# Performance work log

Measured on AMD Instinct MI355X. Metric: run time of the kernel, lower is better.

The kernel has to match this reference:

```python
import jax, jax.numpy as jnp
import numpy as np

B, T, D = 2, 2048, 2048
H, KVH = 32, 8
HD = D // H            # 64
G = H // KVH           # 4


def setup_inputs() -> dict:
    key = jax.random.key(0)
    k1, k2, k3 = jax.random.split(key, 3)
    x_q = jax.random.normal(k1, (B, T, D), dtype=jnp.float32)
    W_qkv = jax.random.normal(k2, (D, H * HD + 2 * KVH * HD), dtype=jnp.float32) * 0.02
    W_out = jax.random.normal(k3, (D, D), dtype=jnp.float32) * 0.02
    b_out = jnp.zeros((D,), dtype=jnp.float32)
    # real rotary tables: theta = 10000^{-2i/HD}
    inv_freq = 1.0 / (10000.0 ** (np.arange(0, HD, 2) / HD))   # [HD/2]
    pos = np.arange(T)[:, None] * inv_freq[None, :]            # [T, HD/2]
    rope_cos = jnp.asarray(np.cos(pos), dtype=jnp.float32)
    rope_sin = jnp.asarray(np.sin(pos), dtype=jnp.float32)
    return {"x_q": x_q, "W_qkv": W_qkv, "W_out": W_out, "b_out": b_out,
            "rope_cos": rope_cos, "rope_sin": rope_sin}


def _apply_rope(x, cos, sin):
    # x: [B, h, T, HD], cos/sin: [T, HD/2] -> interleaved even/odd rotation
    xe = x[..., 0::2]
    xo = x[..., 1::2]
    c = cos[None, None, :, :]
    s = sin[None, None, :, :]
    return jnp.stack([xe * c - xo * s, xe * s + xo * c], axis=-1).reshape(x.shape)


def reference(x_q, W_qkv, W_out, b_out, rope_cos, rope_sin):
    b, t, d = x_q.shape
    qkv = x_q @ W_qkv                                  # [B,T,3072]
    q_lin = qkv[..., : H * HD]
    k_lin = qkv[..., H * HD: H * HD + KVH * HD]
    v_lin = qkv[..., H * HD + KVH * HD:]
    q = q_lin.reshape(b, t, H, HD).transpose(0, 2, 1, 3)        # [B,H,T,HD]
    k = k_lin.reshape(b, t, KVH, HD).transpose(0, 2, 1, 3)      # [B,KVH,T,HD]
    v = v_lin.reshape(b, t, KVH, HD).transpose(0, 2, 1, 3)
    # GQA expand (repeat_interleave over heads)
    k = jnp.repeat(k, G, axis=1)                                # [B,H,T,HD]
    v = jnp.repeat(v, G, axis=1)
    q = _apply_rope(q, rope_cos[:t], rope_sin[:t])
    k = _apply_rope(k, rope_cos[:t], rope_sin[:t])
    scale = 1.0 / jnp.sqrt(jnp.asarray(HD, dtype=x_q.dtype))
    logits = jnp.einsum('bhqd,bhkd->bhqk', q, k) * scale        # [B,H,T,T]
    causal = jnp.triu(jnp.ones((t, t), dtype=bool), 1)[None, None]
    logits = jnp.where(causal, jnp.finfo(logits.dtype).min, logits)
    attn = jax.nn.softmax(logits, axis=-1)
    out = jnp.einsum('bhqk,bhkd->bhqd', attn, v)                # [B,H,T,HD]
    out = out.transpose(0, 2, 1, 3).reshape(b, t, H * HD)       # [B,T,D]
    out = out @ W_out + b_out
    return jnp.nan_to_num(out, nan=0.0, posinf=1e4, neginf=-1e4)
```

## Files before the change

kernel.cpp:

```cpp
#include <hip/hip_runtime.h>
#include <hip/hip_bf16.h>

#define DI __device__ __forceinline__

#if __has_builtin(__builtin_amdgcn_exp2f)
#define EXP2(x) __builtin_amdgcn_exp2f(x)
#else
#define EXP2(x) exp2f(x)
#endif

namespace {

constexpr int Bc = 2, Tc = 2048, Dc = 2048, Hc = 32, KVHc = 8, HDc = 64;
constexpr int NQKV = Hc * HDc + 2 * KVHc * HDc;

typedef __bf16 bf16x8 __attribute__((ext_vector_type(8)));
typedef unsigned short u16x8 __attribute__((ext_vector_type(8)));
typedef unsigned short u16x4 __attribute__((ext_vector_type(4)));
typedef float f32x4 __attribute__((ext_vector_type(4)));

union FragU { u16x8 u; bf16x8 b; u16x4 h[2]; };

DI float bits2f(unsigned int u) {
  union { unsigned int i; float f; } v; v.i = u << 16; return v.f;
}
DI unsigned short f2bits(float f) {
  __hip_bfloat16 h = __float2bfloat16(f);
  return *reinterpret_cast<unsigned short*>(&h);
}

DI void store_out(float* p, float v) { *p = v; }
DI void store_out(__hip_bfloat16* p, float v) { *p = __float2bfloat16(v); }

typedef __attribute__((address_space(1))) void gv_t;
typedef __attribute__((address_space(3))) void lv_t;

template<int ROWB, int TOTB, bool SWZ = false>
DI void stage_tile(const char* g, long long row_stride_b, char* lds) {
  const int tid = threadIdx.x;
  const int wid = tid >> 6, lane = tid & 63;
#pragma unroll
  for (int it = 0; it < TOTB / 4096; ++it) {
    int off = it * 4096 + wid * 1024 + lane * 16;
    int row = off / ROWB;
    int colb = off % ROWB;
    if (SWZ) colb ^= (row & 7) << 4;
    const char* gp = g + (long long)row * row_stride_b + colb;
    char* lp = lds + it * 4096 + wid * 1024;
    __builtin_amdgcn_global_load_lds((gv_t*)gp, (lv_t*)lp, 16, 0, 0);
  }
}

__global__ __launch_bounds__(256) void cvt_f32_bf16(
    const float* __restrict__ in, __hip_bfloat16* __restrict__ out) {
  const long long i = ((long long)blockIdx.x * 256 + threadIdx.x) * 8;
  const float4 a = *(const float4*)(in + i);
  const float4 b = *(const float4*)(in + i + 4);
  u16x8 r;
  r[0] = f2bits(a.x); r[1] = f2bits(a.y); r[2] = f2bits(a.z); r[3] = f2bits(a.w);
  r[4] = f2bits(b.x); r[5] = f2bits(b.y); r[6] = f2bits(b.z); r[7] = f2bits(b.w);
  *(u16x8*)((unsigned short*)out + i) = r;
}

__global__ __launch_bounds__(256) void transpose_cvt_kernel(
    const float* __restrict__ in, __hip_bfloat16* __restrict__ out, int R, int C) {
  __shared__ unsigned short tile[64][65];
  const int c0 = blockIdx.x * 64, r0 = blockIdx.y * 64;
  const int tid = threadIdx.x;
  const int rr = tid >> 2, seg = (tid & 3) * 16;
  const float* src = in + (long long)(r0 + rr) * C + c0 + seg;
#pragma unroll
  for (int i = 0; i < 16; ++i) tile[rr][seg + i] = f2bits(src[i]);
  __syncthreads();
  unsigned short* dst = (unsigned short*)out + (long long)(c0 + rr) * R + r0 + seg;
#pragma unroll
  for (int i = 0; i < 16; ++i) dst[i] = tile[seg + i][rr];
}

__global__ __launch_bounds__(256) void transpose_kernel(
    const __hip_bfloat16* __restrict__ in, __hip_bfloat16* __restrict__ out,
    int R, int C) {
  __shared__ unsigned short tile[64][65];
  const long long slice = (long long)R * C;
  const unsigned short* ip = (const unsigned short*)in + (long long)blockIdx.z * slice;
  unsigned short* op = (unsigned short*)out + (long long)blockIdx.z * slice;
  const int c0 = blockIdx.x * 64, r0 = blockIdx.y * 64;
  const int tid = threadIdx.x;
  const int rr = tid >> 2, seg = (tid & 3) * 16;
  const unsigned short* src = ip + (long long)(r0 + rr) * C + c0 + seg;
#pragma unroll
  for (int i = 0; i < 16; ++i) tile[rr][seg + i] = src[i];
  __syncthreads();
  unsigned short* dst = op + (long long)(c0 + rr) * R + r0 + seg;
#pragma unroll
  for (int i = 0; i < 16; ++i) dst[i] = tile[seg + i][rr];
}

template <typename OT>
__global__ __launch_bounds__(256) void gemm_bt(
    const __hip_bfloat16* __restrict__ A, const __hip_bfloat16* __restrict__ Bt,
    const float* __restrict__ bias, OT* __restrict__ C, int M, int N, int K) {
  __shared__ __align__(16) char As[8192];
  __shared__ __align__(16) char Bs[8192];
  const int n0 = blockIdx.x * 128;
  const int m0 = blockIdx.y * 128;
  const int tid = threadIdx.x;
  const int wid = tid >> 6, lane = tid & 63;
  const int wm = (wid >> 1) * 64, wn = (wid & 1) * 64;
  const int l15 = lane & 15, quad = lane >> 4;

  f32x4 acc[4][4] = {};

  const int nk = K >> 5;
  for (int kt = 0; kt < nk; ++kt) {
    __syncthreads();
    stage_tile<64, 8192>((const char*)(A + (long long)m0 * K + kt * 32), (long long)K * 2, As);
    stage_tile<64, 8192>((const char*)(Bt + (long long)n0 * K + kt * 32), (long long)K * 2, Bs);
    __syncthreads();

    FragU a[4], b[4];
#pragma unroll
    for (int mt = 0; mt < 4; ++mt)
      a[mt].u = *(const u16x8*)(As + ((wm + mt * 16 + l15) * 32 + quad * 8) * 2);
#pragma unroll
    for (int nt = 0; nt < 4; ++nt)
      b[nt].u = *(const u16x8*)(Bs + ((wn + nt * 16 + l15) * 32 + quad * 8) * 2);
#pragma unroll
    for (int mt = 0; mt < 4; ++mt)
#pragma unroll
      for (int nt = 0; nt < 4; ++nt)
        acc[mt][nt] = __builtin_amdgcn_mfma_f32_16x16x32_bf16(a[mt].b, b[nt].b, acc[mt][nt], 0, 0, 0);
  }

#pragma unroll
  for (int nt = 0; nt < 4; ++nt) {
    const int col = n0 + wn + nt * 16 + l15;
    const float bv = bias ? bias[col] : 0.f;
#pragma unroll
    for (int mt = 0; mt < 4; ++mt) {
#pragma unroll
      for (int r = 0; r < 4; ++r) {
        const int row = m0 + wm + mt * 16 + quad * 4 + r;
        store_out(C + (long long)row * N + col, acc[mt][nt][r] + bv);
      }
    }
  }
}

__global__ __launch_bounds__(384) void rope_reshape(
    const __hip_bfloat16* __restrict__ qkv, const float* __restrict__ cosb,
    const float* __restrict__ sinb, __hip_bfloat16* __restrict__ Qo,
    __hip_bfloat16* __restrict__ Ko, __hip_bfloat16* __restrict__ Vo) {
  constexpr float SCL = 0.125f * 1.44269504088896f;
  const int row = blockIdx.x;
  const int b = row / Tc, t = row % Tc;
  const unsigned short* src = (const unsigned short*)qkv + (long long)row * NQKV;
  const float* cb = cosb + t * 32;
  const float* sb = sinb + t * 32;
  const int e = (int)threadIdx.x * 8;
  const u16x8 v = *(const u16x8*)(src + e);
  if (e < Hc * HDc) {
    const int hh = e >> 6, d = e & 63, ii = d >> 1;
    u16x8 r;
#pragma unroll
    for (int p = 0; p < 4; ++p) {
      const float c = cb[ii + p], s = sb[ii + p];
      const float xe = bits2f(v[2 * p]), xo = bits2f(v[2 * p + 1]);
      r[2 * p] = f2bits((xe * c - xo * s) * SCL);
      r[2 * p + 1] = f2bits((xe * s + xo * c) * SCL);
    }
    const long long idx = (((long long)b * Hc + hh) * Tc + t) * HDc + d;
    *(u16x8*)((unsigned short*)Qo + idx) = r;
  } else if (e < Hc * HDc + KVHc * HDc) {
    const int e2 = e - Hc * HDc;
    const int kh = e2 >> 6, d = e2 & 63, ii = d >> 1;
    u16x8 r;
#pragma unroll
    for (int p = 0; p < 4; ++p) {
      const float c = cb[ii + p], s = sb[ii + p];
      const float xe = bits2f(v[2 * p]), xo = bits2f(v[2 * p + 1]);
      r[2 * p] = f2bits(xe * c - xo * s);
      r[2 * p + 1] = f2bits(xe * s + xo * c);
    }
    const long long idx = (((long long)b * KVHc + kh) * Tc + t) * HDc + d;
    *(u16x8*)((unsigned short*)Ko + idx) = r;
  } else {
    const int e2 = e - (Hc * HDc + KVHc * HDc);
    const int kh = e2 >> 6, d = e2 & 63;
    const long long idx = (((long long)b * KVHc + kh) * Tc + t) * HDc + d;
    *(u16x8*)((unsigned short*)Vo + idx) = v;
  }
}


DI void mask_diag(f32x4 (&S)[4], int wid, int l15, int quad) {
#pragma unroll
  for (int nt = 0; nt < 4; ++nt)
#pragma unroll
    for (int r = 0; r < 4; ++r)
      if ((nt * 16 + quad * 4 + r) > (wid * 16 + l15)) S[nt][r] = -1e30f;
}

DI float softmax_pack(f32x4 (&S)[4], float& m_i, float& l_i, FragU (&pa)[2]) {
  float mx = fmaxf(fmaxf(S[0][0], S[0][1]), fmaxf(S[0][2], S[0][3]));
#pragma unroll
  for (int nt = 1; nt < 4; ++nt)
    mx = fmaxf(mx, fmaxf(fmaxf(S[nt][0], S[nt][1]), fmaxf(S[nt][2], S[nt][3])));
  mx = fmaxf(mx, __shfl_xor(mx, 16, 64));
  mx = fmaxf(mx, __shfl_xor(mx, 32, 64));
  const float mnew = fmaxf(m_i, mx);
  const float alpha = EXP2(m_i - mnew);
  m_i = mnew;
  float sum = 0.f;
#pragma unroll
  for (int nt = 0; nt < 4; ++nt)
#pragma unroll
    for (int r = 0; r < 4; ++r) {
      const float pp = EXP2(S[nt][r] - mnew);
      S[nt][r] = pp;
      sum += pp;
    }
  sum += __shfl_xor(sum, 16, 64);
  sum += __shfl_xor(sum, 32, 64);
  l_i = l_i * alpha + sum;
#pragma unroll
  for (int ks = 0; ks < 2; ++ks)
#pragma unroll
    for (int r = 0; r < 4; ++r) {
      pa[ks].u[r] = f2bits(S[2 * ks][r]);
      pa[ks].u[4 + r] = f2bits(S[2 * ks + 1][r]);
    }
  return alpha;
}

DI void attn_tile(const char* __restrict__ Ksb, const char* __restrict__ Vsb,
                  const FragU (&qa)[2], f32x4 (&O)[4], float& m_i, float& l_i,
                  bool diag, int wid, int l15, int quad, int sw) {
  f32x4 S[4] = {};
  __builtin_amdgcn_s_setprio(1);
#pragma unroll
  for (int nt = 0; nt < 4; ++nt) {
#pragma unroll
    for (int ks = 0; ks < 2; ++ks) {
      FragU kb;
      kb.u = *(const u16x8*)(Ksb + (nt * 16 + l15) * 128 + ((((ks << 2) | quad) ^ sw) << 4));
      S[nt] = __builtin_amdgcn_mfma_f32_16x16x32_bf16(kb.b, qa[ks].b, S[nt], 0, 0, 0);
    }
  }
  __builtin_amdgcn_s_setprio(0);
  if (diag) mask_diag(S, wid, l15, quad);
  FragU pa[2];
  const float alpha = softmax_pack(S, m_i, l_i, pa);
#pragma unroll
  for (int nt = 0; nt < 4; ++nt)
#pragma unroll
    for (int r = 0; r < 4; ++r) O[nt][r] *= alpha;
  __builtin_amdgcn_s_setprio(1);
#pragma unroll
  for (int nt = 0; nt < 4; ++nt) {
    const char* vrow = Vsb + (nt * 16 + l15) * 128 + ((quad & 1) << 3);
    const int gq = quad >> 1;
#pragma unroll
    for (int ks = 0; ks < 2; ++ks) {
      FragU vb;
      vb.h[0] = *(const u16x4*)(vrow + (((ks * 4 + gq) ^ sw) << 4));
      vb.h[1] = *(const u16x4*)(vrow + (((ks * 4 + gq + 2) ^ sw) << 4));
      O[nt] = __builtin_amdgcn_mfma_f32_16x16x32_bf16(vb.b, pa[ks].b, O[nt], 0, 0, 0);
    }
  }
  __builtin_amdgcn_s_setprio(0);
}

DI void attn_tile_dual(const char* __restrict__ Ksb, const char* __restrict__ Vsb,
                       const FragU (&qaB)[2], const FragU (&qaA)[2],
                       f32x4 (&OB)[4], f32x4 (&OA)[4],
                       float& mB, float& lB, float& mA, float& lA,
                       bool diagA, int wid, int l15, int quad, int sw) {
  f32x4 SB[4] = {}, SA[4] = {};
  __builtin_amdgcn_s_setprio(1);
#pragma unroll
  for (int nt = 0; nt < 4; ++nt) {
#pragma unroll
    for (int ks = 0; ks < 2; ++ks) {
      FragU kb;
      kb.u = *(const u16x8*)(Ksb + (nt * 16 + l15) * 128 + ((((ks << 2) | quad) ^ sw) << 4));
      SB[nt] = __builtin_amdgcn_mfma_f32_16x16x32_bf16(kb.b, qaB[ks].b, SB[nt], 0, 0, 0);
      SA[nt] = __builtin_amdgcn_mfma_f32_16x16x32_bf16(kb.b, qaA[ks].b, SA[nt], 0, 0, 0);
    }
  }
  __builtin_amdgcn_s_setprio(0);
  if (diagA) mask_diag(SA, wid, l15, quad);
  FragU paB[2], paA[2];
  const float aB = softmax_pack(SB, mB, lB, paB);
  const float aA = softmax_pack(SA, mA, lA, paA);
#pragma unroll
  for (int nt = 0; nt < 4; ++nt)
#pragma unroll
    for (int r = 0; r < 4; ++r) {
      OB[nt][r] *= aB;
      OA[nt][r] *= aA;
    }
  __builtin_amdgcn_s_setprio(1);
#pragma unroll
  for (int nt = 0; nt < 4; ++nt) {
    const char* vrow = Vsb + (nt * 16 + l15) * 128 + ((quad & 1) << 3);
    const int gq = quad >> 1;
#pragma unroll
    for (int ks = 0; ks < 2; ++ks) {
      FragU vb;
      vb.h[0] = *(const u16x4*)(vrow + (((ks * 4 + gq) ^ sw) << 4));
      vb.h[1] = *(const u16x4*)(vrow + (((ks * 4 + gq + 2) ^ sw) << 4));
      OB[nt] = __builtin_amdgcn_mfma_f32_16x16x32_bf16(vb.b, paB[ks].b, OB[nt], 0, 0, 0);
      OA[nt] = __builtin_amdgcn_mfma_f32_16x16x32_bf16(vb.b, paA[ks].b, OA[nt], 0, 0, 0);
    }
  }
  __builtin_amdgcn_s_setprio(0);
}

__global__ __launch_bounds__(256, 4) void attn_kernel(
    const __hip_bfloat16* __restrict__ Q, const __hip_bfloat16* __restrict__ K,
    const __hip_bfloat16* __restrict__ Vt, __hip_bfloat16* __restrict__ Out) {
  __shared__ __align__(16) char Ks[2][8192];
  __shared__ __align__(16) char Vs[2][8192];

  const int p = blockIdx.x;
  const int qtA = p, qtB = (Tc / 64 - 1) - p;
  const int h = blockIdx.y, b = blockIdx.z;
  const int kvh = h >> 2;
  const int tid = threadIdx.x, wid = tid >> 6, lane = tid & 63;
  const int l15 = lane & 15, quad = lane >> 4;
  const int sw = l15 & 7;

  const char* QgA = (const char*)(Q + (((long long)b * Hc + h) * Tc + qtA * 64) * HDc);
  const char* QgB = (const char*)(Q + (((long long)b * Hc + h) * Tc + qtB * 64) * HDc);
  const char* Kg = (const char*)(K + (((long long)b * KVHc + kvh) * Tc) * HDc);
  const char* Vg = (const char*)(Vt + (((long long)b * KVHc + kvh) * HDc) * Tc);

  FragU qaA[2], qaB[2];
#pragma unroll
  for (int ks = 0; ks < 2; ++ks) {
    const int qoff = (wid * 16 + l15) * 128 + (((ks << 2) | quad) << 4);
    qaA[ks].u = *(const u16x8*)(QgA + qoff);
    qaB[ks].u = *(const u16x8*)(QgB + qoff);
  }

  f32x4 OA[4] = {}, OB[4] = {};
  float mA = -1e30f, lA = 0.f, mB = -1e30f, lB = 0.f;

  stage_tile<128, 8192, true>(Kg, 128, Ks[0]);
  stage_tile<128, 8192, true>(Vg, (long long)Tc * 2, Vs[0]);
  asm volatile("s_waitcnt vmcnt(0)" ::: "memory");
  __syncthreads();

  for (int j = 0; j <= qtB; ++j) {
    const int cur = j & 1;
    if (j < qtB) {
      stage_tile<128, 8192, true>(Kg + (long long)(j + 1) * 8192, 128, Ks[cur ^ 1]);
      stage_tile<128, 8192, true>(Vg + (long long)(j + 1) * 128, (long long)Tc * 2, Vs[cur ^ 1]);
    }

    if (j <= qtA) {
      attn_tile_dual(Ks[cur], Vs[cur], qaB, qaA, OB, OA, mB, lB, mA, lA,
                     j == qtA, wid, l15, quad, sw);
    } else {
      attn_tile(Ks[cur], Vs[cur], qaB, OB, mB, lB, j == qtB, wid, l15, quad, sw);
    }

    asm volatile("s_waitcnt vmcnt(0)" ::: "memory");
    __syncthreads();
  }

  const float invA = 1.0f / lA, invB = 1.0f / lB;
  const int tA = qtA * 64 + wid * 16 + l15;
  const int tB = qtB * 64 + wid * 16 + l15;
  unsigned short* obA =
      (unsigned short*)Out + ((long long)b * Tc + tA) * Dc + h * 64 + quad * 4;
  unsigned short* obB =
      (unsigned short*)Out + ((long long)b * Tc + tB) * Dc + h * 64 + quad * 4;
#pragma unroll
  for (int nt = 0; nt < 4; ++nt) {
    u16x4 va, vb;
#pragma unroll
    for (int r = 0; r < 4; ++r) {
      va[r] = f2bits(OA[nt][r] * invA);
      vb[r] = f2bits(OB[nt][r] * invB);
    }
    *(u16x4*)(obA + nt * 16) = va;
    *(u16x4*)(obB + nt * 16) = vb;
  }
}

}

extern "C" void kernel_launch(void* const* d_in, const int* in_sizes, int n_in,
                              void* d_out, int out_size, void* d_ws, size_t ws_size,
                              hipStream_t stream) {
  const float* x_q  = (const float*)d_in[0];
  const float* Wqkv = (const float*)d_in[1];
  const float* Wout = (const float*)d_in[2];
  const float* bout = (const float*)d_in[3];
  const float* rc   = (const float*)d_in[4];
  const float* rs   = (const float*)d_in[5];
  float* out = (float*)d_out;

  constexpr size_t SZ_QKV   = (size_t)Bc * Tc * NQKV * 2;
  constexpr size_t SZ_XB    = (size_t)Bc * Tc * Dc * 2;
  constexpr size_t SZ_QB    = (size_t)Bc * Hc * Tc * HDc * 2;
  constexpr size_t SZ_KV    = (size_t)Bc * KVHc * Tc * HDc * 2;
  constexpr size_t SZ_AO    = (size_t)Bc * Tc * Dc * 2;
  constexpr size_t OFF_QKV   = 0;
  constexpr size_t OFF_XB    = SZ_QKV;
  constexpr size_t OFF_WQKVT = SZ_QKV + SZ_XB;
  constexpr size_t OFF_QB    = SZ_QKV;
  constexpr size_t OFF_KB    = OFF_QB + SZ_QB;
  constexpr size_t OFF_VTMP  = OFF_KB + SZ_KV;
  constexpr size_t OFF_VT    = 0;
  constexpr size_t OFF_AO    = SZ_KV;
  constexpr size_t OFF_WOUTT = OFF_AO + SZ_AO;

  char* w = (char*)d_ws;
  __hip_bfloat16* qkv   = (__hip_bfloat16*)(w + OFF_QKV);
  __hip_bfloat16* xb    = (__hip_bfloat16*)(w + OFF_XB);
  __hip_bfloat16* WqkvT = (__hip_bfloat16*)(w + OFF_WQKVT);
  __hip_bfloat16* Qb    = (__hip_bfloat16*)(w + OFF_QB);
  __hip_bfloat16* Kb    = (__hip_bfloat16*)(w + OFF_KB);
  __hip_bfloat16* Vtmp  = (__hip_bfloat16*)(w + OFF_VTMP);
  __hip_bfloat16* Vt    = (__hip_bfloat16*)(w + OFF_VT);
  __hip_bfloat16* AO    = (__hip_bfloat16*)(w + OFF_AO);
  __hip_bfloat16* WoutT = (__hip_bfloat16*)(w + OFF_WOUTT);

  cvt_f32_bf16<<<dim3((Bc * Tc * Dc) / (256 * 8)), 256, 0, stream>>>(x_q, xb);

  transpose_cvt_kernel<<<dim3(NQKV / 64, Dc / 64), 256, 0, stream>>>(Wqkv, WqkvT, Dc, NQKV);

  gemm_bt<__hip_bfloat16><<<dim3(NQKV / 128, (Bc * Tc) / 128), 256, 0, stream>>>(
      xb, WqkvT, nullptr, qkv, Bc * Tc, NQKV, Dc);

  rope_reshape<<<dim3(Bc * Tc), 384, 0, stream>>>(qkv, rc, rs, Qb, Kb, Vtmp);

  transpose_kernel<<<dim3(HDc / 64, Tc / 64, Bc * KVHc), 256, 0, stream>>>(Vtmp, Vt, Tc, HDc);

  attn_kernel<<<dim3(Tc / 128, Hc, Bc), 256, 0, stream>>>(Qb, Kb, Vt, AO);

  transpose_cvt_kernel<<<dim3(Dc / 64, Dc / 64), 256, 0, stream>>>(Wout, WoutT, Dc, Dc);

  gemm_bt<float><<<dim3(Dc / 128, (Bc * Tc) / 128), 256, 0, stream>>>(
      AO, WoutT, bout, out, Bc * Tc, Dc, Dc);
}
```

Baseline: 349.9 us.

## Deepen GEMM K-tile with swizzled LDS, remap blocks, and lazily rescale softmax

The GEMM now stages 64-wide K slices into XOR-swizzled shared memory and does two MFMA sub-steps per barrier pair, which halves the synchronisation count and is meant to cut LDS bank conflicts. Block IDs are also remapped in groups of eight to change the tile-to-workgroup assignment, likely for cache locality across dies. In attention, the online softmax skips the max update and the O/l rescale unless some lane's new max exceeds the running max by more than 8 (in exp2 units). This trades bounded growth of the exponentials for fewer multiplies, with a small overflow risk for bf16 P values.

```diff
diff --git a/kernel.cpp b/kernel.cpp
--- a/kernel.cpp
+++ b/kernel.cpp
@@ -100,36 +100,50 @@
 __global__ __launch_bounds__(256) void gemm_bt(
     const __hip_bfloat16* __restrict__ A, const __hip_bfloat16* __restrict__ Bt,
     const float* __restrict__ bias, OT* __restrict__ C, int M, int N, int K) {
-  __shared__ __align__(16) char As[8192];
-  __shared__ __align__(16) char Bs[8192];
-  const int n0 = blockIdx.x * 128;
-  const int m0 = blockIdx.y * 128;
+  __shared__ __align__(16) char As[16384];
+  __shared__ __align__(16) char Bs[16384];
+  const int nwgx = N >> 7;
+  const int nwg = nwgx * (M >> 7);
+  const int bid0 = blockIdx.y * nwgx + blockIdx.x;
+  const int cpx = nwg >> 3;
+  const int bid = (bid0 & 7) * cpx + (bid0 >> 3);
+  const int n0 = (bid % nwgx) * 128;
+  const int m0 = (bid / nwgx) * 128;
   const int tid = threadIdx.x;
   const int wid = tid >> 6, lane = tid & 63;
   const int wm = (wid >> 1) * 64, wn = (wid & 1) * 64;
   const int l15 = lane & 15, quad = lane >> 4;
+  const int sw = l15 & 7;
 
   f32x4 acc[4][4] = {};
 
-  const int nk = K >> 5;
+  const int nk = K >> 6;
   for (int kt = 0; kt < nk; ++kt) {
     __syncthreads();
-    stage_tile<64, 8192>((const char*)(A + (long long)m0 * K + kt * 32), (long long)K * 2, As);
-    stage_tile<64, 8192>((const char*)(Bt + (long long)n0 * K + kt * 32), (long long)K * 2, Bs);
+    stage_tile<128, 16384, true>((const char*)(A + (long long)m0 * K + kt * 64),
+                                 (long long)K * 2, As);
+    stage_tile<128, 16384, true>((const char*)(Bt + (long long)n0 * K + kt * 64),
+                                 (long long)K * 2, Bs);
     __syncthreads();
 
-    FragU a[4], b[4];
-#pragma unroll
-    for (int mt = 0; mt < 4; ++mt)
-      a[mt].u = *(const u16x8*)(As + ((wm + mt * 16 + l15) * 32 + quad * 8) * 2);
-#pragma unroll
-    for (int nt = 0; nt < 4; ++nt)
-      b[nt].u = *(const u16x8*)(Bs + ((wn + nt * 16 + l15) * 32 + quad * 8) * 2);
-#pragma unroll
-    for (int mt = 0; mt < 4; ++mt)
+#pragma unroll
+    for (int kk = 0; kk < 2; ++kk) {
+      FragU a[4], b[4];
+#pragma unroll
+      for (int mt = 0; mt < 4; ++mt)
+        a[mt].u = *(const u16x8*)(As + (wm + mt * 16 + l15) * 128 +
+                                  ((((kk << 2) | quad) ^ sw) << 4));
 #pragma unroll
       for (int nt = 0; nt < 4; ++nt)
-        acc[mt][nt] = __builtin_amdgcn_mfma_f32_16x16x32_bf16(a[mt].b, b[nt].b, acc[mt][nt], 0, 0, 0);
+        b[nt].u = *(const u16x8*)(Bs + (wn + nt * 16 + l15) * 128 +
+                                  ((((kk << 2) | quad) ^ sw) << 4));
+#pragma unroll
+      for (int mt = 0; mt < 4; ++mt)
+#pragma unroll
+        for (int nt = 0; nt < 4; ++nt)
+          acc[mt][nt] =
+              __builtin_amdgcn_mfma_f32_16x16x32_bf16(a[mt].b, b[nt].b, acc[mt][nt], 0, 0, 0);
+    }
   }
 
 #pragma unroll
@@ -201,28 +215,36 @@
       if ((nt * 16 + quad * 4 + r) > (wid * 16 + l15)) S[nt][r] = -1e30f;
 }
 
-DI float softmax_pack(f32x4 (&S)[4], float& m_i, float& l_i, FragU (&pa)[2]) {
+DI void softmax_update(f32x4 (&S)[4], f32x4 (&O)[4], float& m_i, float& l_i,
+                       FragU (&pa)[2]) {
   float mx = fmaxf(fmaxf(S[0][0], S[0][1]), fmaxf(S[0][2], S[0][3]));
 #pragma unroll
   for (int nt = 1; nt < 4; ++nt)
     mx = fmaxf(mx, fmaxf(fmaxf(S[nt][0], S[nt][1]), fmaxf(S[nt][2], S[nt][3])));
   mx = fmaxf(mx, __shfl_xor(mx, 16, 64));
   mx = fmaxf(mx, __shfl_xor(mx, 32, 64));
-  const float mnew = fmaxf(m_i, mx);
-  const float alpha = EXP2(m_i - mnew);
-  m_i = mnew;
+  if (!__all(mx <= m_i + 8.f)) {
+    const float mnew = fmaxf(m_i, mx);
+    const float alpha = EXP2(m_i - mnew);
+    m_i = mnew;
+    l_i *= alpha;
+#pragma unroll
+    for (int nt = 0; nt < 4; ++nt)
+#pragma unroll
+      for (int r = 0; r < 4; ++r) O[nt][r] *= alpha;
+  }
   float sum = 0.f;
 #pragma unroll
   for (int nt = 0; nt < 4; ++nt)
 #pragma unroll
     for (int r = 0; r < 4; ++r) {
-      const float pp = EXP2(S[nt][r] - mnew);
+      const float pp = EXP2(S[nt][r] - m_i);
       S[nt][r] = pp;
       sum += pp;
     }
   sum += __shfl_xor(sum, 16, 64);
   sum += __shfl_xor(sum, 32, 64);
-  l_i = l_i * alpha + sum;
+  l_i += sum;
 #pragma unroll
   for (int ks = 0; ks < 2; ++ks)
 #pragma unroll
@@ -230,7 +252,6 @@
       pa[ks].u[r] = f2bits(S[2 * ks][r]);
       pa[ks].u[4 + r] = f2bits(S[2 * ks + 1][r]);
     }
-  return alpha;
 }
 
 DI void attn_tile(const char* __restrict__ Ksb, const char* __restrict__ Vsb,
@@ -250,11 +271,7 @@
   __builtin_amdgcn_s_setprio(0);
   if (diag) mask_diag(S, wid, l15, quad);
   FragU pa[2];
-  const float alpha = softmax_pack(S, m_i, l_i, pa);
-#pragma unroll
-  for (int nt = 0; nt < 4; ++nt)
-#pragma unroll
-    for (int r = 0; r < 4; ++r) O[nt][r] *= alpha;
+  softmax_update(S, O, m_i, l_i, pa);
   __builtin_amdgcn_s_setprio(1);
 #pragma unroll
   for (int nt = 0; nt < 4; ++nt) {
@@ -291,15 +308,8 @@
   __builtin_amdgcn_s_setprio(0);
   if (diagA) mask_diag(SA, wid, l15, quad);
   FragU paB[2], paA[2];
-  const float aB = softmax_pack(SB, mB, lB, paB);
-  const float aA = softmax_pack(SA, mA, lA, paA);
-#pragma unroll
-  for (int nt = 0; nt < 4; ++nt)
-#pragma unroll
-    for (int r = 0; r < 4; ++r) {
-      OB[nt][r] *= aB;
-      OA[nt][r] *= aA;
-    }
+  softmax_update(SB, OB, mB, lB, paB);
+  softmax_update(SA, OA, mA, lA, paA);
   __builtin_amdgcn_s_setprio(1);
 #pragma unroll
   for (int nt = 0; nt < 4; ++nt) {
```

Result: faster. 330.6 us (-5.5%).
